# Performance work log

Hardware: AMD Instinct MI355X
Metric: run time of the kernel (lower is better)

The kernel has to match this reference:

```python
import jax, jax.numpy as jnp
import numpy as np

B, S, D = 4, 2048, 1024
H, HD = 16, 64
WINDOW = 256


def setup_inputs() -> dict:
    key = jax.random.key(0)
    ks = jax.random.split(key, 5)
    scale = 1.0 / np.sqrt(D)
    return {
        "hidden_states": jax.random.normal(ks[0], (B, S, D), dtype=jnp.float32),
        "Wq": jax.random.normal(ks[1], (D, D), dtype=jnp.float32) * scale,
        "Wk": jax.random.normal(ks[2], (D, D), dtype=jnp.float32) * scale,
        "Wv": jax.random.normal(ks[3], (D, D), dtype=jnp.float32) * scale,
        "Wo": jax.random.normal(ks[4], (D, D), dtype=jnp.float32) * scale,
        "bo": jnp.zeros((D,), dtype=jnp.float32),
    }


def reference(hidden_states, Wq, Wk, Wv, Wo, bo):
    # q/k/v projections (no bias), torch Linear: x @ W.T
    q = hidden_states @ Wq.T  # [B,S,D]
    k = hidden_states @ Wk.T
    v = hidden_states @ Wv.T

    def split_heads(t):  # [B,S,D] -> [B,H,S,HD]
        return t.reshape(B, S, H, HD).transpose(0, 2, 1, 3)

    q, k, v = split_heads(q), split_heads(k), split_heads(v)

    # NOTE: original code does NOT scale by 1/sqrt(head_dim)
    scores = jnp.einsum("bhqd,bhkd->bhqk", q.astype(jnp.float32), k.astype(jnp.float32))

    # local causal band mask: keep j <= i and i - j < WINDOW
    i = jnp.arange(S)[:, None]
    j = jnp.arange(S)[None, :]
    band = (j <= i) & (i - j < WINDOW)  # [S,S] bool
    mask_value = jnp.finfo(scores.dtype).min
    scores = jnp.where(band[None, None, :, :], scores, mask_value)

    attn = jax.nn.softmax(scores, axis=-1).astype(v.dtype)
    ctx = jnp.einsum("bhqk,bhkd->bhqd", attn, v)  # [B,H,S,HD]

    # merge heads -> [B,S,D]
    ctx = ctx.transpose(0, 2, 1, 3).reshape(B, S, D)
    out = ctx @ Wo.T + bo
    return out
```

## Files before the change

kernel.cpp:

```cpp
#include <hip/hip_runtime.h>
#include <hip/hip_bf16.h>
#include <cstdint>
#include <cstddef>

#define S_LEN   2048
#define BATCH   4
#define NHEAD   16
#define HDIM    64
#define DMODEL  1024
#define WIN     256
#define PQ      72

typedef __bf16 bf16x8 __attribute__((ext_vector_type(8)));
typedef float f32x4 __attribute__((ext_vector_type(4)));
typedef unsigned short u16x4 __attribute__((ext_vector_type(4)));
typedef unsigned short u16x8 __attribute__((ext_vector_type(8)));

__device__ __forceinline__ unsigned short f2bf(float x) {
  union { float f; unsigned u; } c; c.f = x;
  unsigned r = (c.u + 0x7fffu + ((c.u >> 16) & 1u)) >> 16;
  return (unsigned short)r;
}

__device__ __forceinline__ void gld_lds16(const void* g, void* l) {
  __builtin_amdgcn_global_load_lds(
      (__attribute__((address_space(1))) void*)g,
      (__attribute__((address_space(3))) void*)l, 16, 0, 0);
}

__global__ __launch_bounds__(256) void convert_kernel(
    const float* __restrict__ s0, const float* __restrict__ s1,
    const float* __restrict__ s2, const float* __restrict__ s3,
    const float* __restrict__ s4,
    unsigned short* __restrict__ d0, unsigned short* __restrict__ d1,
    unsigned short* __restrict__ d2, unsigned short* __restrict__ d3,
    unsigned short* __restrict__ d4) {
  const int z = blockIdx.y;
  const float* s; unsigned short* d; long n;
  if      (z == 0) { s = s0; d = d0; n = (long)8192 * 1024; }
  else if (z == 1) { s = s1; d = d1; n = (long)1024 * 1024; }
  else if (z == 2) { s = s2; d = d2; n = (long)1024 * 1024; }
  else if (z == 3) { s = s3; d = d3; n = (long)1024 * 1024; }
  else             { s = s4; d = d4; n = (long)1024 * 1024; }
  const long base = ((long)blockIdx.x * 256 + threadIdx.x) * 16;
  if (base >= n) return;
#pragma unroll
  for (int i = 0; i < 4; ++i) {
    const float4 f = *(const float4*)(s + base + i * 4);
    u16x4 ov;
    ov.x = f2bf(f.x); ov.y = f2bf(f.y); ov.z = f2bf(f.z); ov.w = f2bf(f.w);
    *(u16x4*)(d + base + i * 4) = ov;
  }
}

template <int MODE>
__device__ __forceinline__ void gemm_bt_core(
    const unsigned short* __restrict__ A, const unsigned short* __restrict__ B,
    void* __restrict__ C, const float* __restrict__ bias,
    int M, int N, int K) {
  const int m0 = blockIdx.x * 128;
  const int n0 = blockIdx.y * 128;
  const int tid  = threadIdx.x;
  const int wave = tid >> 6, lane = tid & 63;
  const int quad = lane >> 4, l16 = lane & 15;
  const int wm = wave >> 1, wn = wave & 1;

  __shared__ unsigned short lsA[128 * 32];
  __shared__ unsigned short lsB[128 * 32];

  f32x4 acc[4][4];
#pragma unroll
  for (int i = 0; i < 4; ++i)
#pragma unroll
    for (int j = 0; j < 4; ++j) acc[i][j] = f32x4{0.f, 0.f, 0.f, 0.f};

  const int arow = tid >> 2;
  const int acol = (tid & 3) * 8;
  const int swz_s = ((arow >> 1) & 3) << 3;
  const int swz_r = ((l16 >> 1) & 3) << 3;

  for (int k0 = 0; k0 < K; k0 += 32) {
    __syncthreads();
#pragma unroll
    for (int r = 0; r < 2; ++r) {
      const int row  = arow + r * 64;
      const int flat = row * 32 + acol;
      gld_lds16(A + (size_t)(m0 + row) * K + k0 + (acol ^ swz_s), lsA + flat);
      gld_lds16(B + (size_t)(n0 + row) * K + k0 + (acol ^ swz_s), lsB + flat);
    }
    __syncthreads();

    bf16x8 af[4], bfr[4];
#pragma unroll
    for (int mi = 0; mi < 4; ++mi)
      af[mi] = *(const bf16x8*)(lsA + (wm * 64 + mi * 16 + l16) * 32 + ((quad * 8) ^ swz_r));
#pragma unroll
    for (int ni = 0; ni < 4; ++ni)
      bfr[ni] = *(const bf16x8*)(lsB + (wn * 64 + ni * 16 + l16) * 32 + ((quad * 8) ^ swz_r));
#pragma unroll
    for (int mi = 0; mi < 4; ++mi)
#pragma unroll
      for (int ni = 0; ni < 4; ++ni)
        acc[mi][ni] = __builtin_amdgcn_mfma_f32_16x16x32_bf16(
            af[mi], bfr[ni], acc[mi][ni], 0, 0, 0);
  }

#pragma unroll
  for (int mi = 0; mi < 4; ++mi) {
#pragma unroll
    for (int r = 0; r < 4; ++r) {
      const int m = m0 + wm * 64 + mi * 16 + quad * 4 + r;
#pragma unroll
      for (int ni = 0; ni < 4; ++ni) {
        const int n = n0 + wn * 64 + ni * 16 + l16;
        const float vv = acc[mi][ni][r];
        if (MODE == 0) {
          ((unsigned short*)C)[(size_t)m * N + n] = f2bf(vv);
        } else {
          ((float*)C)[(size_t)m * N + n] = vv + bias[n];
        }
      }
    }
  }
}

__global__ __launch_bounds__(256) void gemm_qkv_kernel(
    const unsigned short* __restrict__ A,
    const unsigned short* __restrict__ B0, const unsigned short* __restrict__ B1,
    const unsigned short* __restrict__ B2,
    unsigned short* __restrict__ C0, unsigned short* __restrict__ C1,
    unsigned short* __restrict__ C2, int M, int N, int K) {
  const unsigned short* B = blockIdx.z == 0 ? B0 : (blockIdx.z == 1 ? B1 : B2);
  unsigned short*       C = blockIdx.z == 0 ? C0 : (blockIdx.z == 1 ? C1 : C2);
  gemm_bt_core<0>(A, B, C, nullptr, M, N, K);
}

__global__ __launch_bounds__(256) void gemm_out_kernel(
    const unsigned short* __restrict__ A, const unsigned short* __restrict__ B,
    float* __restrict__ C, const float* __restrict__ bias, int M, int N, int K) {
  gemm_bt_core<1>(A, B, C, bias, M, N, K);
}

__global__ __launch_bounds__(256) void transpose_v_kernel(
    const unsigned short* __restrict__ v, unsigned short* __restrict__ vt) {
  const int bh = blockIdx.y;
  const int b = bh >> 4, h = bh & 15;
  const int s0 = blockIdx.x * 64;
  __shared__ unsigned short t[64][PQ];
  const int r = threadIdx.x >> 2, cb = (threadIdx.x & 3) * 16;
  const unsigned short* src =
      v + ((size_t)(b * S_LEN + s0 + r) * DMODEL + h * HDIM + cb);
  *(u16x8*)(&t[r][cb])     = *(const u16x8*)src;
  *(u16x8*)(&t[r][cb + 8]) = *(const u16x8*)(src + 8);
  __syncthreads();
  const int d = threadIdx.x >> 2, sc = (threadIdx.x & 3) * 16;
  u16x8 o0, o1;
#pragma unroll
  for (int jj = 0; jj < 8; ++jj) { o0[jj] = t[sc + jj][d]; o1[jj] = t[sc + 8 + jj][d]; }
  unsigned short* dst = vt + ((size_t)(bh * HDIM + d) * S_LEN + s0 + sc);
  *(u16x8*)dst       = o0;
  *(u16x8*)(dst + 8) = o1;
}

__global__ __launch_bounds__(256) void attn_kernel(
    const unsigned short* __restrict__ q, const unsigned short* __restrict__ k,
    const unsigned short* __restrict__ vt, unsigned short* __restrict__ ctx) {
  const int bh = blockIdx.y;
  const int b = bh >> 4, h = bh & 15;
  const int i0 = blockIdx.x * 64;
  const int tid  = threadIdx.x;
  const int wave = tid >> 6, lane = tid & 63;
  const int quad = lane >> 4, l16 = lane & 15;

  __shared__ unsigned short lsQ[64 * PQ];
  __shared__ unsigned short lsK[64 * PQ];
  __shared__ unsigned short lsV[64 * PQ];
  __shared__ unsigned short lsP[4][16 * PQ];

  {
    const int r = tid >> 2, cb = (tid & 3) * 16;
    const unsigned short* src =
        q + ((size_t)(b * S_LEN + i0 + r) * DMODEL + h * HDIM + cb);
    *(u16x8*)(lsQ + r * PQ + cb)     = *(const u16x8*)src;
    *(u16x8*)(lsQ + r * PQ + cb + 8) = *(const u16x8*)(src + 8);
  }
  __syncthreads();

  bf16x8 aq[2];
#pragma unroll
  for (int s2 = 0; s2 < 2; ++s2)
    aq[s2] = *(const bf16x8*)(lsQ + (wave * 16 + l16) * PQ + s2 * 32 + quad * 8);

  float m_i[4], l_i[4];
  f32x4 o[4];
#pragma unroll
  for (int r = 0; r < 4; ++r) { m_i[r] = -1e30f; l_i[r] = 0.f; }
#pragma unroll
  for (int ni = 0; ni < 4; ++ni) o[ni] = f32x4{0.f, 0.f, 0.f, 0.f};

  const int jb0 = (i0 >= WIN ? (i0 - WIN + 1) : 0) >> 6;
  const int jb1 = i0 >> 6;

  for (int jb = jb0; jb <= jb1; ++jb) {
    const int j0 = jb * 64;
    const bool needMask = (jb == jb1) || (jb + 3 < jb1);
    __syncthreads();
    {
      const int r = tid >> 2, cb = (tid & 3) * 16;
      const unsigned short* ks =
          k + ((size_t)(b * S_LEN + j0 + r) * DMODEL + h * HDIM + cb);
      *(u16x8*)(lsK + r * PQ + cb)     = *(const u16x8*)ks;
      *(u16x8*)(lsK + r * PQ + cb + 8) = *(const u16x8*)(ks + 8);
      const unsigned short* vs =
          vt + ((size_t)(bh * HDIM + r) * S_LEN + j0 + cb);
      *(u16x8*)(lsV + r * PQ + cb)     = *(const u16x8*)vs;
      *(u16x8*)(lsV + r * PQ + cb + 8) = *(const u16x8*)(vs + 8);
    }
    __syncthreads();

    f32x4 s[4];
#pragma unroll
    for (int ni = 0; ni < 4; ++ni) s[ni] = f32x4{0.f, 0.f, 0.f, 0.f};
#pragma unroll
    for (int s2 = 0; s2 < 2; ++s2) {
#pragma unroll
      for (int ni = 0; ni < 4; ++ni) {
        const bf16x8 bk = *(const bf16x8*)(lsK + (ni * 16 + l16) * PQ + s2 * 32 + quad * 8);
        s[ni] = __builtin_amdgcn_mfma_f32_16x16x32_bf16(aq[s2], bk, s[ni], 0, 0, 0);
      }
    }

    float mnew[4], alpha[4], rsum[4];
#pragma unroll
    for (int r = 0; r < 4; ++r) mnew[r] = m_i[r];

    if (needMask) {
#pragma unroll
      for (int ni = 0; ni < 4; ++ni)
#pragma unroll
        for (int r = 0; r < 4; ++r) {
          const int i = i0 + wave * 16 + quad * 4 + r;
          const int j = j0 + ni * 16 + l16;
          const bool ok = (j <= i) && (i - j < WIN);
          const float val = ok ? s[ni][r] : -1e30f;
          s[ni][r] = val;
          mnew[r] = fmaxf(mnew[r], val);
        }
    } else {
#pragma unroll
      for (int ni = 0; ni < 4; ++ni)
#pragma unroll
        for (int r = 0; r < 4; ++r) mnew[r] = fmaxf(mnew[r], s[ni][r]);
    }
#pragma unroll
    for (int off = 1; off < 16; off <<= 1)
#pragma unroll
      for (int r = 0; r < 4; ++r)
        mnew[r] = fmaxf(mnew[r], __shfl_xor(mnew[r], off, 64));

#pragma unroll
    for (int r = 0; r < 4; ++r) {
      alpha[r] = __expf(m_i[r] - mnew[r]);
      rsum[r] = 0.f;
      m_i[r] = mnew[r];
    }

#pragma unroll
    for (int ni = 0; ni < 4; ++ni)
#pragma unroll
      for (int r = 0; r < 4; ++r) {
        const float p = __expf(s[ni][r] - mnew[r]);
        rsum[r] += p;
        lsP[wave][(quad * 4 + r) * PQ + ni * 16 + l16] = f2bf(p);
      }
#pragma unroll
    for (int off = 1; off < 16; off <<= 1)
#pragma unroll
      for (int r = 0; r < 4; ++r)
        rsum[r] += __shfl_xor(rsum[r], off, 64);

#pragma unroll
    for (int r = 0; r < 4; ++r)
      l_i[r] = l_i[r] * alpha[r] + rsum[r];
#pragma unroll
    for (int ni = 0; ni < 4; ++ni)
#pragma unroll
      for (int r = 0; r < 4; ++r)
        o[ni][r] *= alpha[r];

    __builtin_amdgcn_s_waitcnt(0);

#pragma unroll
    for (int s2 = 0; s2 < 2; ++s2) {
      const bf16x8 ap = *(const bf16x8*)(lsP[wave] + l16 * PQ + s2 * 32 + quad * 8);
#pragma unroll
      for (int ni = 0; ni < 4; ++ni) {
        const bf16x8 bv = *(const bf16x8*)(lsV + (ni * 16 + l16) * PQ + s2 * 32 + quad * 8);
        o[ni] = __builtin_amdgcn_mfma_f32_16x16x32_bf16(ap, bv, o[ni], 0, 0, 0);
      }
    }
  }

#pragma unroll
  for (int r = 0; r < 4; ++r) {
    const int i = i0 + wave * 16 + quad * 4 + r;
    const float inv = 1.f / l_i[r];
#pragma unroll
    for (int ni = 0; ni < 4; ++ni)
      ctx[(size_t)(b * S_LEN + i) * DMODEL + h * HDIM + ni * 16 + l16] =
          f2bf(o[ni][r] * inv);
  }
}

extern "C" void kernel_launch(void* const* d_in, const int* in_sizes, int n_in,
                              void* d_out, int out_size, void* d_ws, size_t ws_size,
                              hipStream_t stream) {
  const float* hs = (const float*)d_in[0];
  const float* Wq = (const float*)d_in[1];
  const float* Wk = (const float*)d_in[2];
  const float* Wv = (const float*)d_in[3];
  const float* Wo = (const float*)d_in[4];
  const float* bo = (const float*)d_in[5];
  float* out = (float*)d_out;

  const size_t MD = (size_t)8192 * 1024;
  const size_t DD = (size_t)1024 * 1024;
  unsigned short* hsb  = (unsigned short*)d_ws;
  unsigned short* wqb  = hsb + MD;
  unsigned short* wkb  = wqb + DD;
  unsigned short* wvb  = wkb + DD;
  unsigned short* wob  = wvb + DD;
  unsigned short* qb   = wob + DD;
  unsigned short* kb   = qb + MD;
  unsigned short* vb   = kb + MD;
  unsigned short* ctxb = vb + MD;
  unsigned short* vtb  = ctxb + MD;

  convert_kernel<<<dim3(2048, 5), 256, 0, stream>>>(hs, Wq, Wk, Wv, Wo,
                                                    hsb, wqb, wkb, wvb, wob);
  gemm_qkv_kernel<<<dim3(64, 8, 3), 256, 0, stream>>>(hsb, wqb, wkb, wvb,
                                                      qb, kb, vb, 8192, 1024, 1024);
  transpose_v_kernel<<<dim3(32, 64), 256, 0, stream>>>(vb, vtb);
  attn_kernel<<<dim3(32, 64), 256, 0, stream>>>(qb, kb, vtb, ctxb);
  gemm_out_kernel<<<dim3(64, 8), 256, 0, stream>>>(ctxb, wob, out, bo,
                                                   8192, 1024, 1024);
}
```

Baseline: 238.4 us.

## Deepen GEMM K-tile to 64 and restructure attention into register-resident transposed-score tiles

The GEMM core now stages 64-wide K slices with an 8-chunk XOR swizzle, which halves the number of barrier-separated iterations. The attention kernel handles 128 queries per block, with each wave owning two 16-row query tiles. It computes S^T = K·Q^T so that the probabilities come out in MFMA A-operand layout and can be packed straight from registers, removing the per-wave LDS round-trip for P and its waitcnt. The V tile is permuted on load so that this register layout lines up. These changes are meant to cut LDS traffic and synchronisation and to reuse each K/V tile across more queries, at the cost of more register pressure and fewer attention blocks.

```diff
diff --git a/kernel.cpp b/kernel.cpp
--- a/kernel.cpp
+++ b/kernel.cpp
@@ -65,8 +65,8 @@
   const int quad = lane >> 4, l16 = lane & 15;
   const int wm = wave >> 1, wn = wave & 1;
 
-  __shared__ unsigned short lsA[128 * 32];
-  __shared__ unsigned short lsB[128 * 32];
+  __shared__ unsigned short lsA[128 * 64];
+  __shared__ unsigned short lsB[128 * 64];
 
   f32x4 acc[4][4];
 #pragma unroll
@@ -74,35 +74,41 @@
 #pragma unroll
     for (int j = 0; j < 4; ++j) acc[i][j] = f32x4{0.f, 0.f, 0.f, 0.f};
 
-  const int arow = tid >> 2;
-  const int acol = (tid & 3) * 8;
-  const int swz_s = ((arow >> 1) & 3) << 3;
-  const int swz_r = ((l16 >> 1) & 3) << 3;
-
-  for (int k0 = 0; k0 < K; k0 += 32) {
+  const int trow   = tid >> 3;
+  const int tchunk = tid & 7;
+  const int swz_w  = (trow >> 1) & 7;
+  const int scol   = ((tchunk ^ swz_w) << 3);
+  const int swz_r  = (l16 >> 1) & 7;
+
+  for (int k0 = 0; k0 < K; k0 += 64) {
     __syncthreads();
 #pragma unroll
-    for (int r = 0; r < 2; ++r) {
-      const int row  = arow + r * 64;
-      const int flat = row * 32 + acol;
-      gld_lds16(A + (size_t)(m0 + row) * K + k0 + (acol ^ swz_s), lsA + flat);
-      gld_lds16(B + (size_t)(n0 + row) * K + k0 + (acol ^ swz_s), lsB + flat);
+    for (int c = 0; c < 4; ++c) {
+      const int row  = trow + 32 * c;
+      const int flat = row * 64 + tchunk * 8;
+      gld_lds16(A + (size_t)(m0 + row) * K + k0 + scol, lsA + flat);
+      gld_lds16(B + (size_t)(n0 + row) * K + k0 + scol, lsB + flat);
     }
     __syncthreads();
 
-    bf16x8 af[4], bfr[4];
-#pragma unroll
-    for (int mi = 0; mi < 4; ++mi)
-      af[mi] = *(const bf16x8*)(lsA + (wm * 64 + mi * 16 + l16) * 32 + ((quad * 8) ^ swz_r));
-#pragma unroll
-    for (int ni = 0; ni < 4; ++ni)
-      bfr[ni] = *(const bf16x8*)(lsB + (wn * 64 + ni * 16 + l16) * 32 + ((quad * 8) ^ swz_r));
-#pragma unroll
-    for (int mi = 0; mi < 4; ++mi)
+#pragma unroll
+    for (int s2 = 0; s2 < 2; ++s2) {
+      bf16x8 af[4], bfr[4];
+#pragma unroll
+      for (int mi = 0; mi < 4; ++mi)
+        af[mi] = *(const bf16x8*)(lsA + (wm * 64 + mi * 16 + l16) * 64 +
+                                  (((s2 * 4 + quad) ^ swz_r) << 3));
 #pragma unroll
       for (int ni = 0; ni < 4; ++ni)
-        acc[mi][ni] = __builtin_amdgcn_mfma_f32_16x16x32_bf16(
-            af[mi], bfr[ni], acc[mi][ni], 0, 0, 0);
+        bfr[ni] = *(const bf16x8*)(lsB + (wn * 64 + ni * 16 + l16) * 64 +
+                                   (((s2 * 4 + quad) ^ swz_r) << 3));
+#pragma unroll
+      for (int mi = 0; mi < 4; ++mi)
+#pragma unroll
+        for (int ni = 0; ni < 4; ++ni)
+          acc[mi][ni] = __builtin_amdgcn_mfma_f32_16x16x32_bf16(
+              af[mi], bfr[ni], acc[mi][ni], 0, 0, 0);
+    }
   }
 
 #pragma unroll
@@ -167,43 +173,50 @@
     const unsigned short* __restrict__ vt, unsigned short* __restrict__ ctx) {
   const int bh = blockIdx.y;
   const int b = bh >> 4, h = bh & 15;
-  const int i0 = blockIdx.x * 64;
+  const int i0 = blockIdx.x * 128;
   const int tid  = threadIdx.x;
   const int wave = tid >> 6, lane = tid & 63;
   const int quad = lane >> 4, l16 = lane & 15;
 
-  __shared__ unsigned short lsQ[64 * PQ];
+  __shared__ unsigned short lsQ[128 * PQ];
   __shared__ unsigned short lsK[64 * PQ];
-  __shared__ unsigned short lsV[64 * PQ];
-  __shared__ unsigned short lsP[4][16 * PQ];
+  __shared__ unsigned short lsVp[64 * PQ];
 
   {
-    const int r = tid >> 2, cb = (tid & 3) * 16;
+    const int r = tid >> 1, cb = (tid & 1) * 32;
     const unsigned short* src =
         q + ((size_t)(b * S_LEN + i0 + r) * DMODEL + h * HDIM + cb);
-    *(u16x8*)(lsQ + r * PQ + cb)     = *(const u16x8*)src;
-    *(u16x8*)(lsQ + r * PQ + cb + 8) = *(const u16x8*)(src + 8);
+    *(u16x8*)(lsQ + r * PQ + cb)      = *(const u16x8*)src;
+    *(u16x8*)(lsQ + r * PQ + cb + 8)  = *(const u16x8*)(src + 8);
+    *(u16x8*)(lsQ + r * PQ + cb + 16) = *(const u16x8*)(src + 16);
+    *(u16x8*)(lsQ + r * PQ + cb + 24) = *(const u16x8*)(src + 24);
   }
   __syncthreads();
 
-  bf16x8 aq[2];
-#pragma unroll
-  for (int s2 = 0; s2 < 2; ++s2)
-    aq[s2] = *(const bf16x8*)(lsQ + (wave * 16 + l16) * PQ + s2 * 32 + quad * 8);
-
-  float m_i[4], l_i[4];
-  f32x4 o[4];
-#pragma unroll
-  for (int r = 0; r < 4; ++r) { m_i[r] = -1e30f; l_i[r] = 0.f; }
-#pragma unroll
-  for (int ni = 0; ni < 4; ++ni) o[ni] = f32x4{0.f, 0.f, 0.f, 0.f};
-
-  const int jb0 = (i0 >= WIN ? (i0 - WIN + 1) : 0) >> 6;
-  const int jb1 = i0 >> 6;
+  bf16x8 aq[2][2];
+#pragma unroll
+  for (int t = 0; t < 2; ++t)
+#pragma unroll
+    for (int s2 = 0; s2 < 2; ++s2)
+      aq[t][s2] = *(const bf16x8*)(lsQ + (wave * 32 + t * 16 + l16) * PQ +
+                                   s2 * 32 + quad * 8);
+
+  float m_s[2], l_s[2];
+  f32x4 o[2][4];
+#pragma unroll
+  for (int t = 0; t < 2; ++t) { m_s[t] = -1e30f; l_s[t] = 0.f; }
+#pragma unroll
+  for (int t = 0; t < 2; ++t)
+#pragma unroll
+    for (int nd = 0; nd < 4; ++nd) o[t][nd] = f32x4{0.f, 0.f, 0.f, 0.f};
+
+  const int jb0 = (i0 >= WIN) ? ((i0 - WIN + 1) >> 6) : 0;
+  const int jb1 = (i0 + 127) >> 6;
+  const int jbi = i0 >> 6;
 
   for (int jb = jb0; jb <= jb1; ++jb) {
     const int j0 = jb * 64;
-    const bool needMask = (jb == jb1) || (jb + 3 < jb1);
+    const bool needMask = !(jb == jbi - 1 || jb == jbi - 2);
     __syncthreads();
     {
       const int r = tid >> 2, cb = (tid & 3) * 16;
@@ -213,102 +226,132 @@
       *(u16x8*)(lsK + r * PQ + cb + 8) = *(const u16x8*)(ks + 8);
       const unsigned short* vs =
           vt + ((size_t)(bh * HDIM + r) * S_LEN + j0 + cb);
-      *(u16x8*)(lsV + r * PQ + cb)     = *(const u16x8*)vs;
-      *(u16x8*)(lsV + r * PQ + cb + 8) = *(const u16x8*)(vs + 8);
+      const u16x8 va = *(const u16x8*)vs;
+      const u16x8 vb = *(const u16x8*)(vs + 8);
+      const int jhi = cb >> 4;
+      const int base = (jhi >> 1) * 32 + (jhi & 1) * 4;
+      u16x4 w0, w1, w2, w3;
+      w0[0]=va[0];  w0[1]=va[1];  w0[2]=va[2];  w0[3]=va[3];
+      w1[0]=va[4];  w1[1]=va[5];  w1[2]=va[6];  w1[3]=va[7];
+      w2[0]=vb[0];  w2[1]=vb[1];  w2[2]=vb[2];  w2[3]=vb[3];
+      w3[0]=vb[4];  w3[1]=vb[5];  w3[2]=vb[6];  w3[3]=vb[7];
+      *(u16x4*)(lsVp + r * PQ + base)      = w0;
+      *(u16x4*)(lsVp + r * PQ + base + 8)  = w1;
+      *(u16x4*)(lsVp + r * PQ + base + 16) = w2;
+      *(u16x4*)(lsVp + r * PQ + base + 24) = w3;
     }
     __syncthreads();
 
-    f32x4 s[4];
-#pragma unroll
-    for (int ni = 0; ni < 4; ++ni) s[ni] = f32x4{0.f, 0.f, 0.f, 0.f};
+    f32x4 st[2][4];
+#pragma unroll
+    for (int t = 0; t < 2; ++t)
+#pragma unroll
+      for (int ni = 0; ni < 4; ++ni) st[t][ni] = f32x4{0.f, 0.f, 0.f, 0.f};
 #pragma unroll
     for (int s2 = 0; s2 < 2; ++s2) {
-#pragma unroll
-      for (int ni = 0; ni < 4; ++ni) {
-        const bf16x8 bk = *(const bf16x8*)(lsK + (ni * 16 + l16) * PQ + s2 * 32 + quad * 8);
-        s[ni] = __builtin_amdgcn_mfma_f32_16x16x32_bf16(aq[s2], bk, s[ni], 0, 0, 0);
+      bf16x8 bk[4];
+#pragma unroll
+      for (int ni = 0; ni < 4; ++ni)
+        bk[ni] = *(const bf16x8*)(lsK + (ni * 16 + l16) * PQ + s2 * 32 + quad * 8);
+#pragma unroll
+      for (int t = 0; t < 2; ++t)
+#pragma unroll
+        for (int ni = 0; ni < 4; ++ni)
+          st[t][ni] = __builtin_amdgcn_mfma_f32_16x16x32_bf16(
+              bk[ni], aq[t][s2], st[t][ni], 0, 0, 0);
+    }
+
+    bf16x8 ap[2][2];
+    float alpha_o[2][4];
+#pragma unroll
+    for (int t = 0; t < 2; ++t) {
+      const int iq = i0 + wave * 32 + t * 16 + l16;
+      float mloc = -1e30f;
+      if (needMask) {
+#pragma unroll
+        for (int ni = 0; ni < 4; ++ni)
+#pragma unroll
+          for (int r = 0; r < 4; ++r) {
+            const int j = j0 + ni * 16 + quad * 4 + r;
+            const bool ok = (j <= iq) && (iq - j < WIN);
+            const float val = ok ? st[t][ni][r] : -1e30f;
+            st[t][ni][r] = val;
+            mloc = fmaxf(mloc, val);
+          }
+      } else {
+#pragma unroll
+        for (int ni = 0; ni < 4; ++ni)
+#pragma unroll
+          for (int r = 0; r < 4; ++r) mloc = fmaxf(mloc, st[t][ni][r]);
       }
-    }
-
-    float mnew[4], alpha[4], rsum[4];
-#pragma unroll
-    for (int r = 0; r < 4; ++r) mnew[r] = m_i[r];
-
-    if (needMask) {
+      mloc = fmaxf(mloc, __shfl_xor(mloc, 16, 64));
+      mloc = fmaxf(mloc, __shfl_xor(mloc, 32, 64));
+      const float mnew = fmaxf(m_s[t], mloc);
+      const float alpha = __expf(m_s[t] - mnew);
+      m_s[t] = mnew;
+
+      float rs = 0.f;
 #pragma unroll
       for (int ni = 0; ni < 4; ++ni)
 #pragma unroll
         for (int r = 0; r < 4; ++r) {
-          const int i = i0 + wave * 16 + quad * 4 + r;
-          const int j = j0 + ni * 16 + l16;
-          const bool ok = (j <= i) && (i - j < WIN);
-          const float val = ok ? s[ni][r] : -1e30f;
-          s[ni][r] = val;
-          mnew[r] = fmaxf(mnew[r], val);
+          const float p = __expf(st[t][ni][r] - mnew);
+          st[t][ni][r] = p;
+          rs += p;
         }
-    } else {
-#pragma unroll
-      for (int ni = 0; ni < 4; ++ni)
-#pragma unroll
-        for (int r = 0; r < 4; ++r) mnew[r] = fmaxf(mnew[r], s[ni][r]);
-    }
-#pragma unroll
-    for (int off = 1; off < 16; off <<= 1)
+      rs += __shfl_xor(rs, 16, 64);
+      rs += __shfl_xor(rs, 32, 64);
+      l_s[t] = l_s[t] * alpha + rs;
+
+#pragma unroll
+      for (int s2 = 0; s2 < 2; ++s2) {
+        bf16x8 a;
+#pragma unroll
+        for (int r = 0; r < 4; ++r) {
+          union { unsigned short u; __bf16 h; } c0, c1;
+          c0.u = f2bf(st[t][2 * s2][r]);
+          c1.u = f2bf(st[t][2 * s2 + 1][r]);
+          a[r]     = c0.h;
+          a[4 + r] = c1.h;
+        }
+        ap[t][s2] = a;
+      }
 #pragma unroll
       for (int r = 0; r < 4; ++r)
-        mnew[r] = fmaxf(mnew[r], __shfl_xor(mnew[r], off, 64));
-
+        alpha_o[t][r] = __shfl(alpha, quad * 4 + r, 64);
+#pragma unroll
+      for (int nd = 0; nd < 4; ++nd)
+#pragma unroll
+        for (int r = 0; r < 4; ++r) o[t][nd][r] *= alpha_o[t][r];
+    }
+
+#pragma unroll
+    for (int s2 = 0; s2 < 2; ++s2) {
+      bf16x8 bv[4];
+#pragma unroll
+      for (int nd = 0; nd < 4; ++nd)
+        bv[nd] = *(const bf16x8*)(lsVp + (nd * 16 + l16) * PQ + s2 * 32 + quad * 8);
+#pragma unroll
+      for (int t = 0; t < 2; ++t)
+#pragma unroll
+        for (int nd = 0; nd < 4; ++nd)
+          o[t][nd] = __builtin_amdgcn_mfma_f32_16x16x32_bf16(
+              ap[t][s2], bv[nd], o[t][nd], 0, 0, 0);
+    }
+  }
+
+#pragma unroll
+  for (int t = 0; t < 2; ++t) {
+    const float invl = 1.f / l_s[t];
 #pragma unroll
     for (int r = 0; r < 4; ++r) {
-      alpha[r] = __expf(m_i[r] - mnew[r]);
-      rsum[r] = 0.f;
-      m_i[r] = mnew[r];
-    }
-
-#pragma unroll
-    for (int ni = 0; ni < 4; ++ni)
-#pragma unroll
-      for (int r = 0; r < 4; ++r) {
-        const float p = __expf(s[ni][r] - mnew[r]);
-        rsum[r] += p;
-        lsP[wave][(quad * 4 + r) * PQ + ni * 16 + l16] = f2bf(p);
-      }
-#pragma unroll
-    for (int off = 1; off < 16; off <<= 1)
-#pragma unroll
-      for (int r = 0; r < 4; ++r)
-        rsum[r] += __shfl_xor(rsum[r], off, 64);
-
-#pragma unroll
-    for (int r = 0; r < 4; ++r)
-      l_i[r] = l_i[r] * alpha[r] + rsum[r];
-#pragma unroll
-    for (int ni = 0; ni < 4; ++ni)
-#pragma unroll
-      for (int r = 0; r < 4; ++r)
-        o[ni][r] *= alpha[r];
-
-    __builtin_amdgcn_s_waitcnt(0);
-
-#pragma unroll
-    for (int s2 = 0; s2 < 2; ++s2) {
-      const bf16x8 ap = *(const bf16x8*)(lsP[wave] + l16 * PQ + s2 * 32 + quad * 8);
-#pragma unroll
-      for (int ni = 0; ni < 4; ++ni) {
-        const bf16x8 bv = *(const bf16x8*)(lsV + (ni * 16 + l16) * PQ + s2 * 32 + quad * 8);
-        o[ni] = __builtin_amdgcn_mfma_f32_16x16x32_bf16(ap, bv, o[ni], 0, 0, 0);
-      }
-    }
-  }
-
-#pragma unroll
-  for (int r = 0; r < 4; ++r) {
-    const int i = i0 + wave * 16 + quad * 4 + r;
-    const float inv = 1.f / l_i[r];
-#pragma unroll
-    for (int ni = 0; ni < 4; ++ni)
-      ctx[(size_t)(b * S_LEN + i) * DMODEL + h * HDIM + ni * 16 + l16] =
-          f2bf(o[ni][r] * inv);
+      const float inv = __shfl(invl, quad * 4 + r, 64);
+      const int i = i0 + wave * 32 + t * 16 + quad * 4 + r;
+#pragma unroll
+      for (int nd = 0; nd < 4; ++nd)
+        ctx[(size_t)(b * S_LEN + i) * DMODEL + h * HDIM + nd * 16 + l16] =
+            f2bf(o[t][nd][r] * inv);
+    }
   }
 }
 
@@ -341,7 +384,7 @@
   gemm_qkv_kernel<<<dim3(64, 8, 3), 256, 0, stream>>>(hsb, wqb, wkb, wvb,
                                                       qb, kb, vb, 8192, 1024, 1024);
   transpose_v_kernel<<<dim3(32, 64), 256, 0, stream>>>(vb, vtb);
-  attn_kernel<<<dim3(32, 64), 256, 0, stream>>>(qb, kb, vtb, ctxb);
+  attn_kernel<<<dim3(16, 64), 256, 0, stream>>>(qb, kb, vtb, ctxb);
   gemm_out_kernel<<<dim3(64, 8), 256, 0, stream>>>(ctxb, wob, out, bo,
                                                    8192, 1024, 1024);
 }
```

Result: faster. 229.2 us (-3.8%).
